# Kernel optimization log

Hardware: AMD Instinct MI355X
Metric: run time of the kernel (lower is better)

## Reference

```python
import jax, jax.numpy as jnp
import numpy as np

N_NODES = 100_000
N_EDGES = 1_600_000
N_GRAPHS = 256
IN_DIM, HID, HEADS, LAYERS = 480, 128, 4, 3
HEAD_DIM = HID // HEADS
NEG_SLOPE = 0.2
LN_EPS = 1e-5


def setup_inputs() -> dict:
    key = jax.random.key(0)
    ks = jax.random.split(key, 12)
    x = jax.random.normal(ks[0], (N_NODES, IN_DIM), dtype=jnp.float32)
    edge_index = jax.random.randint(ks[1], (2, N_EDGES), 0, N_NODES, dtype=jnp.int32)
    batch = jnp.sort(jax.random.randint(ks[2], (N_NODES,), 0, N_GRAPHS, dtype=jnp.int32))
    s_in = 1.0 / np.sqrt(IN_DIM)
    s_h = 1.0 / np.sqrt(HID)
    return {
        "x": x,
        "W_in": jax.random.uniform(ks[3], (IN_DIM, HID), jnp.float32, -s_in, s_in),
        "b_in": jax.random.uniform(ks[4], (HID,), jnp.float32, -s_in, s_in),
        "W_gat": jax.random.uniform(ks[5], (LAYERS, HID, HID), jnp.float32, -s_h, s_h),
        "att_src": jax.random.uniform(ks[6], (LAYERS, HEADS, HEAD_DIM), jnp.float32, -s_h, s_h),
        "att_dst": jax.random.uniform(ks[7], (LAYERS, HEADS, HEAD_DIM), jnp.float32, -s_h, s_h),
        "b_gat": jnp.zeros((LAYERS, HID), jnp.float32),
        "ln_g": jnp.ones((LAYERS, HID), jnp.float32),
        "ln_b": jnp.zeros((LAYERS, HID), jnp.float32),
        "edge_index": edge_index,
        "batch": batch,
    }


def _gat_conv(h_in, W, a_src, a_dst, bias, src, dst, n):
    # h: [N, H, D] per-head projected features
    h = (h_in @ W).reshape(n, HEADS, HEAD_DIM)
    asrc = jnp.sum(h * a_src, axis=-1)  # [N, H]
    adst = jnp.sum(h * a_dst, axis=-1)  # [N, H]
    e = jax.nn.leaky_relu(asrc[src] + adst[dst], NEG_SLOPE)  # [E, H]
    # scatter-softmax over incoming edges of each destination node
    emax = jax.ops.segment_max(e, dst, num_segments=n)  # [N, H]
    emax = jnp.where(jnp.isfinite(emax), emax, 0.0)
    ex = jnp.exp(e - emax[dst])
    denom = jax.ops.segment_sum(ex, dst, num_segments=n)
    alpha = ex / jnp.maximum(denom, 1e-16)[dst]  # [E, H]
    out = jax.ops.segment_sum(alpha[:, :, None] * h[src], dst, num_segments=n)
    return out.reshape(n, HID) + bias


def _layer_norm(x, g, b):
    mu = jnp.mean(x, axis=-1, keepdims=True)
    var = jnp.mean(jnp.square(x - mu), axis=-1, keepdims=True)
    return (x - mu) * jax.lax.rsqrt(var + LN_EPS) * g + b


def reference(x, W_in, b_in, W_gat, att_src, att_dst, b_gat, ln_g, ln_b, edge_index, batch):
    n = x.shape[0]
    # PyG GATConv default add_self_loops=True
    loop = jnp.arange(n, dtype=edge_index.dtype)
    src = jnp.concatenate([edge_index[0], loop])
    dst = jnp.concatenate([edge_index[1], loop])

    h = jax.nn.relu(x @ W_in + b_in)
    for l in range(LAYERS):
        residual = h
        h = _gat_conv(h, W_gat[l], att_src[l], att_dst[l], b_gat[l], src, dst, n)
        h = jax.nn.relu(_layer_norm(h, ln_g[l], ln_b[l]))
        # dropout omitted (eval mode)
        h = h + residual
    # global mean pool per graph
    sums = jax.ops.segment_sum(h, batch, num_segments=N_GRAPHS)
    cnt = jax.ops.segment_sum(jnp.ones((n,), h.dtype), batch, num_segments=N_GRAPHS)
    return sums / jnp.maximum(cnt, 1.0)[:, None]
```

## Files before the change

kernel.cpp:

```cpp
#include <hip/hip_runtime.h>
#include <hip/hip_bf16.h>

#define HID 128
#define NEG_SLOPE 0.2f
#define LN_EPS 1e-5f
#define SEG_CAP 8192

typedef __attribute__((ext_vector_type(8))) short short8;
typedef __attribute__((ext_vector_type(4))) float floatx4;

__device__ __forceinline__ float us2f(unsigned short u) {
    union { unsigned int i; float f; } c; c.i = ((unsigned int)u) << 16; return c.f;
}
__device__ __forceinline__ float lo2f(unsigned u) {
    union { unsigned int i; float f; } c; c.i = u << 16; return c.f;
}
__device__ __forceinline__ float hi2f(unsigned u) {
    union { unsigned int i; float f; } c; c.i = u & 0xffff0000u; return c.f;
}
__device__ __forceinline__ unsigned short f2us(float f) {
    union { float f; unsigned u; } c; c.f = f;
    unsigned r = c.u + 0x7FFF + ((c.u >> 16) & 1);
    return (unsigned short)(r >> 16);
}
__device__ __forceinline__ unsigned pack2(float a, float b) {
    return (unsigned)f2us(a) | ((unsigned)f2us(b) << 16);
}
__device__ __forceinline__ float ldw(const void* p, long i, int bf) {
    return bf ? us2f(((const unsigned short*)p)[i]) : ((const float*)p)[i];
}
__device__ __forceinline__ float lrelu(float x) { return x > 0.f ? x : NEG_SLOPE * x; }
__device__ __forceinline__ float wsum(float x) {
#pragma unroll
    for (int o = 32; o > 0; o >>= 1) x += __shfl_xor(x, o);
    return x;
}
__device__ __forceinline__ float pick4(float4 v, int h) {
    return h == 0 ? v.x : (h == 1 ? v.y : (h == 2 ? v.z : v.w));
}

__global__ void detect_kernel(const float* __restrict__ x, int* __restrict__ flag) {
    float v = x[threadIdx.x];
    int bad = (!(v == v)) || (fabsf(v) > 1e6f);
    unsigned long long m = __ballot(bad);
    if (threadIdx.x == 0) flag[0] = (m != 0ull) ? 1 : 0;
}

__global__ __launch_bounds__(256) void zero_int_kernel(int* p, int n) {
    int i = blockIdx.x * 256 + threadIdx.x;
    if (i < n) p[i] = 0;
}

__global__ __launch_bounds__(256) void bucket_hist_kernel(const int* __restrict__ dst, int E, int nb,
                                                          int* __restrict__ bucket_cnt) {
    __shared__ int hist[512];
    for (int i = threadIdx.x; i < nb; i += 256) hist[i] = 0;
    __syncthreads();
    const int base = blockIdx.x * 4096;
    const int end = min(base + 4096, E);
    for (int i = base + threadIdx.x; i < end; i += 256)
        atomicAdd(&hist[dst[i] >> 8], 1);
    __syncthreads();
    for (int i = threadIdx.x; i < nb; i += 256)
        if (hist[i]) atomicAdd(&bucket_cnt[i], hist[i]);
}

__global__ __launch_bounds__(512) void bucket_scan_kernel(const int* __restrict__ bucket_cnt,
                                                          int* __restrict__ bucket_base,
                                                          int* __restrict__ cursor,
                                                          int nb, int* __restrict__ row_ptr, int N) {
    __shared__ int sc[512];
    const int t = threadIdx.x;
    const int v = (t < nb) ? bucket_cnt[t] : 0;
    int x = v;
    sc[t] = x;
    __syncthreads();
    for (int o = 1; o < 512; o <<= 1) {
        const int y = (t >= o) ? sc[t - o] : 0;
        __syncthreads();
        x += y;
        sc[t] = x;
        __syncthreads();
    }
    if (t < nb) { bucket_base[t] = x - v; cursor[t] = x - v; }
    if (t == nb - 1) { bucket_base[nb] = x; row_ptr[N] = x; }
}

__global__ __launch_bounds__(256) void partition_kernel(const int* __restrict__ src, const int* __restrict__ dst,
                                                        int E, int nb, int* __restrict__ cursor,
                                                        unsigned long long* __restrict__ tmp) {
    __shared__ int hist[512];
    __shared__ int tbase[512];
    for (int i = threadIdx.x; i < nb; i += 256) hist[i] = 0;
    __syncthreads();
    const int base = blockIdx.x * 4096;
    const int end = min(base + 4096, E);
    int myd[16], mys[16], myr[16];
#pragma unroll
    for (int j = 0; j < 16; ++j) {
        const int i = base + threadIdx.x + j * 256;
        if (i < end) {
            const int d = dst[i];
            myd[j] = d;
            mys[j] = src[i];
            myr[j] = atomicAdd(&hist[d >> 8], 1);
        } else {
            myd[j] = -1;
        }
    }
    __syncthreads();
    for (int i = threadIdx.x; i < nb; i += 256) {
        const int hv = hist[i];
        tbase[i] = hv ? atomicAdd(&cursor[i], hv) : 0;
    }
    __syncthreads();
#pragma unroll
    for (int j = 0; j < 16; ++j) {
        if (myd[j] >= 0) {
            const int b = myd[j] >> 8;
            tmp[(size_t)tbase[b] + myr[j]] = ((unsigned long long)(unsigned)myd[j] << 32) | (unsigned)mys[j];
        }
    }
}

__global__ __launch_bounds__(256) void bucket_sort_kernel(const unsigned long long* __restrict__ tmp,
                                                          const int* __restrict__ bucket_base,
                                                          int* __restrict__ row_ptr, int* __restrict__ csr,
                                                          int N) {
    __shared__ int hist[256];
    __shared__ int sc[256];
    __shared__ int off[256];
    __shared__ int outb[SEG_CAP];
    const int b = blockIdx.x;
    const int node0 = b << 8;
    const int nn = min(256, N - node0);
    const int s0 = bucket_base[b], s1 = bucket_base[b + 1];
    const int cnt = s1 - s0;
    const int t = threadIdx.x;
    hist[t] = 0;
    __syncthreads();
    for (int i = s0 + t; i < s1; i += 256) {
        const int d = (int)(tmp[i] >> 32) - node0;
        atomicAdd(&hist[d], 1);
    }
    __syncthreads();
    const int v = hist[t];
    int x = v;
    sc[t] = x;
    __syncthreads();
    for (int o = 1; o < 256; o <<= 1) {
        const int y = (t >= o) ? sc[t - o] : 0;
        __syncthreads();
        x += y;
        sc[t] = x;
        __syncthreads();
    }
    off[t] = x - v;
    if (t < nn) row_ptr[node0 + t] = s0 + (x - v);
    hist[t] = 0;
    __syncthreads();
    if (cnt <= SEG_CAP) {
        for (int i = s0 + t; i < s1; i += 256) {
            const unsigned long long pr = tmp[i];
            const int d = (int)(pr >> 32) - node0;
            const int p = off[d] + atomicAdd(&hist[d], 1);
            outb[p] = (int)(unsigned)(pr & 0xffffffffu);
        }
        __syncthreads();
        for (int i = t; i < cnt; i += 256) csr[s0 + i] = outb[i];
    } else {
        for (int i = s0 + t; i < s1; i += 256) {
            const unsigned long long pr = tmp[i];
            const int d = (int)(pr >> 32) - node0;
            const int p = off[d] + atomicAdd(&hist[d], 1);
            csr[s0 + p] = (int)(unsigned)(pr & 0xffffffffu);
        }
    }
}

__global__ __launch_bounds__(256) void transpose_w_kernel(const void* __restrict__ W, long w_off, int K,
                                                          unsigned short* __restrict__ Wt,
                                                          const int* __restrict__ flagp) {
    const int bf = flagp[0];
    const int i = blockIdx.x * 256 + threadIdx.x;
    if (i >= 128 * K) return;
    const int n = i / K, k = i - n * K;
    const long s = w_off + (long)k * 128 + n;
    Wt[i] = bf ? ((const unsigned short*)W)[s] : f2us(((const float*)W)[s]);
}

template <int C_BF>
__global__ __launch_bounds__(256) void mfma_gemm_kernel(const void* __restrict__ Ap, int a_input,
                                                        const unsigned short* __restrict__ Bt,
                                                        const void* __restrict__ bias, long bias_off,
                                                        void* __restrict__ Cp,
                                                        int M, int K, int do_relu,
                                                        const int* __restrict__ flagp) {
    __shared__ unsigned short As[128 * 40];
    __shared__ unsigned short Bs[128 * 40];
    const int bf = flagp[0];
    const int a_bf = a_input ? bf : 2;
    const int t = threadIdx.x;
    const int bm = blockIdx.x * 128;
    const int lane = t & 63, wave = t >> 6;
    const int r = lane & 15, quad = lane >> 4;
    const int srow = t >> 1, skh = (t & 1) * 16;

    floatx4 acc[2][8];
#pragma unroll
    for (int mt = 0; mt < 2; ++mt)
#pragma unroll
        for (int nt = 0; nt < 8; ++nt)
#pragma unroll
            for (int q = 0; q < 4; ++q) acc[mt][nt][q] = 0.f;

    for (int k0 = 0; k0 < K; k0 += 32) {
        {
            const int grow = bm + srow;
            uint4 u0 = make_uint4(0, 0, 0, 0), u1 = u0;
            if (grow < M) {
                const long aidx = (long)grow * K + k0 + skh;
                if (a_bf == 1) {
                    const unsigned short* ap = (const unsigned short*)Ap + aidx;
                    u0 = ((const uint4*)ap)[0];
                    u1 = ((const uint4*)ap)[1];
                } else {
                    const float* ap = (const float*)Ap + aidx;
                    float4 f0 = ((const float4*)ap)[0];
                    float4 f1 = ((const float4*)ap)[1];
                    float4 f2 = ((const float4*)ap)[2];
                    float4 f3 = ((const float4*)ap)[3];
                    u0 = make_uint4(pack2(f0.x, f0.y), pack2(f0.z, f0.w), pack2(f1.x, f1.y), pack2(f1.z, f1.w));
                    u1 = make_uint4(pack2(f2.x, f2.y), pack2(f2.z, f2.w), pack2(f3.x, f3.y), pack2(f3.z, f3.w));
                }
            }
            *(uint4*)&As[srow * 40 + skh]     = u0;
            *(uint4*)&As[srow * 40 + skh + 8] = u1;
        }
        {
            const unsigned short* bp = Bt + (long)srow * K + k0 + skh;
            uint4 v0 = ((const uint4*)bp)[0];
            uint4 v1 = ((const uint4*)bp)[1];
            *(uint4*)&Bs[srow * 40 + skh]     = v0;
            *(uint4*)&Bs[srow * 40 + skh + 8] = v1;
        }
        __syncthreads();

        short8 afr[2];
        afr[0] = *(const short8*)&As[(wave * 32 + r) * 40 + quad * 8];
        afr[1] = *(const short8*)&As[(wave * 32 + 16 + r) * 40 + quad * 8];
#pragma unroll
        for (int nt = 0; nt < 8; ++nt) {
            short8 bfr = *(const short8*)&Bs[(nt * 16 + r) * 40 + quad * 8];
            acc[0][nt] = __builtin_amdgcn_mfma_f32_16x16x32_bf16(afr[0], bfr, acc[0][nt], 0, 0, 0);
            acc[1][nt] = __builtin_amdgcn_mfma_f32_16x16x32_bf16(afr[1], bfr, acc[1][nt], 0, 0, 0);
        }
        __syncthreads();
    }

    float bb[8];
#pragma unroll
    for (int nt = 0; nt < 8; ++nt) bb[nt] = bias ? ldw(bias, bias_off + nt * 16 + r, bf) : 0.f;

#pragma unroll
    for (int mt = 0; mt < 2; ++mt) {
        const int gr0 = bm + wave * 32 + mt * 16 + quad * 4;
#pragma unroll
        for (int reg = 0; reg < 4; ++reg) {
            const int grow = gr0 + reg;
            if (grow < M) {
#pragma unroll
                for (int nt = 0; nt < 8; ++nt) {
                    float v = acc[mt][nt][reg] + bb[nt];
                    if (do_relu) v = fmaxf(v, 0.f);
                    const long ci = (long)grow * HID + nt * 16 + r;
                    if (C_BF) ((unsigned short*)Cp)[ci] = f2us(v);
                    else      ((float*)Cp)[ci] = v;
                }
            }
        }
    }
}

__global__ __launch_bounds__(256) void attn_kernel(const unsigned short* __restrict__ hp,
                                                   const void* __restrict__ att_src,
                                                   const void* __restrict__ att_dst, long a_off,
                                                   float* __restrict__ asrc, float* __restrict__ adst,
                                                   int N, const int* __restrict__ flagp) {
    __shared__ float sA[128], sD[128];
    const int bf = flagp[0];
    const int t = threadIdx.x;
    if (t < 128) { sA[t] = ldw(att_src, a_off + t, bf); sD[t] = ldw(att_dst, a_off + t, bf); }
    __syncthreads();
    const int gid = blockIdx.x * 256 + t;
    if (gid >= N * 4) return;
    const int n = gid >> 2, hd = gid & 3;
    const unsigned short* p = hp + (size_t)n * HID + hd * 32;
    float s1 = 0.f, s2 = 0.f;
#pragma unroll
    for (int q = 0; q < 4; ++q) {
        uint4 v = ((const uint4*)p)[q];
        unsigned arr[4] = {v.x, v.y, v.z, v.w};
#pragma unroll
        for (int j = 0; j < 4; ++j) {
            const int k = q * 8 + j * 2;
            float lo = lo2f(arr[j]);
            float hi = hi2f(arr[j]);
            s1 += lo * sA[hd * 32 + k] + hi * sA[hd * 32 + k + 1];
            s2 += lo * sD[hd * 32 + k] + hi * sD[hd * 32 + k + 1];
        }
    }
    asrc[gid] = s1;
    adst[gid] = s2;
}

__global__ __launch_bounds__(256) void gat_kernel(float* __restrict__ h,
                                                  const unsigned short* __restrict__ hp,
                                                  const float* __restrict__ asrc,
                                                  const float* __restrict__ adst,
                                                  const int* __restrict__ row_ptr,
                                                  const int* __restrict__ csr,
                                                  const void* __restrict__ bgat,
                                                  const void* __restrict__ lng,
                                                  const void* __restrict__ lnb, long w_off,
                                                  int N, const int* __restrict__ flagp) {
    __shared__ uint2 ebuf[4][320];
    const int bf = flagp[0];
    const int lane = threadIdx.x & 63;
    const int wslot = threadIdx.x >> 6;
    const int half = lane >> 5;
    const int ll = lane & 31;
    const int head4 = ll >> 3;
    const int c0 = ll << 2;
    const int n = (blockIdx.x << 2) | wslot;
    if (n >= N) return;

    const int e0 = row_ptr[n], e1 = row_ptr[n + 1];
    const float4 ad4 = *(const float4*)(adst + (size_t)n * 4);
    const float4 as4 = *(const float4*)(asrc + (size_t)n * 4);
    float4 es;
    es.x = lrelu(as4.x + ad4.x); es.y = lrelu(as4.y + ad4.y);
    es.z = lrelu(as4.z + ad4.z); es.w = lrelu(as4.w + ad4.w);

    const uint2 us = *(const uint2*)(hp + (size_t)n * HID + c0);
    const float wself = half ? 0.f : 1.f;
    float4 acc;
    acc.x = wself * lo2f(us.x); acc.y = wself * hi2f(us.x);
    acc.z = wself * lo2f(us.y); acc.w = wself * hi2f(us.y);

    float4 dnp = make_float4(0.f, 0.f, 0.f, 0.f);
    uint2* eb = ebuf[wslot];

    for (int base = e0; base < e1; base += 64) {
        const int cnt = min(64, e1 - base);
        int s = 0;
        float4 ex4 = make_float4(0.f, 0.f, 0.f, 0.f);
        if (lane < cnt) {
            s = csr[base + lane];
            const float4 a = *(const float4*)(asrc + (size_t)s * 4);
            ex4.x = __expf(lrelu(a.x + ad4.x) - es.x);
            ex4.y = __expf(lrelu(a.y + ad4.y) - es.y);
            ex4.z = __expf(lrelu(a.z + ad4.z) - es.z);
            ex4.w = __expf(lrelu(a.w + ad4.w) - es.w);
            dnp.x += ex4.x; dnp.y += ex4.y; dnp.z += ex4.z; dnp.w += ex4.w;
        }
        const unsigned su = (unsigned)s;
        eb[lane * 5 + 0] = make_uint2(su, __float_as_uint(ex4.x));
        eb[lane * 5 + 1] = make_uint2(su, __float_as_uint(ex4.y));
        eb[lane * 5 + 2] = make_uint2(su, __float_as_uint(ex4.z));
        eb[lane * 5 + 3] = make_uint2(su, __float_as_uint(ex4.w));

        float4 aA = make_float4(0.f, 0.f, 0.f, 0.f);
        float4 aB = make_float4(0.f, 0.f, 0.f, 0.f);
        int i = half;
#define GAT_EDGE(idx, A)                                                      \
        {                                                                     \
            const uint2 q = eb[(idx) * 5 + head4];                            \
            const uint2 u = *(const uint2*)(hp + (size_t)q.x * HID + c0);     \
            const float wq = __uint_as_float(q.y);                            \
            A.x = fmaf(wq, lo2f(u.x), A.x);                                   \
            A.y = fmaf(wq, hi2f(u.x), A.y);                                   \
            A.z = fmaf(wq, lo2f(u.y), A.z);                                   \
            A.w = fmaf(wq, hi2f(u.y), A.w);                                   \
        }
        for (; i + 2 < cnt; i += 4) {
            GAT_EDGE(i, aA);
            GAT_EDGE(i + 2, aB);
        }
        for (; i < cnt; i += 2) GAT_EDGE(i, aA);
#undef GAT_EDGE
        acc.x += aA.x + aB.x; acc.y += aA.y + aB.y;
        acc.z += aA.z + aB.z; acc.w += aA.w + aB.w;
    }

    acc.x += __shfl_xor(acc.x, 32);
    acc.y += __shfl_xor(acc.y, 32);
    acc.z += __shfl_xor(acc.z, 32);
    acc.w += __shfl_xor(acc.w, 32);

    float4 dn;
    dn.x = wsum(dnp.x) + 1.f;
    dn.y = wsum(dnp.y) + 1.f;
    dn.z = wsum(dnp.z) + 1.f;
    dn.w = wsum(dnp.w) + 1.f;

    const float invd = 1.f / fmaxf(pick4(dn, head4), 1e-16f);
    acc.x *= invd; acc.y *= invd; acc.z *= invd; acc.w *= invd;
    acc.x += ldw(bgat, w_off + c0 + 0, bf);
    acc.y += ldw(bgat, w_off + c0 + 1, bf);
    acc.z += ldw(bgat, w_off + c0 + 2, bf);
    acc.w += ldw(bgat, w_off + c0 + 3, bf);

    const float mean = wsum(acc.x + acc.y + acc.z + acc.w) * (1.f / 256.f);
    const float d0 = acc.x - mean, d1 = acc.y - mean, d2 = acc.z - mean, d3 = acc.w - mean;
    const float var = wsum(d0 * d0 + d1 * d1 + d2 * d2 + d3 * d3) * (1.f / 256.f);
    const float rstd = rsqrtf(var + LN_EPS);
    float o0 = d0 * rstd * ldw(lng, w_off + c0 + 0, bf) + ldw(lnb, w_off + c0 + 0, bf);
    float o1 = d1 * rstd * ldw(lng, w_off + c0 + 1, bf) + ldw(lnb, w_off + c0 + 1, bf);
    float o2 = d2 * rstd * ldw(lng, w_off + c0 + 2, bf) + ldw(lnb, w_off + c0 + 2, bf);
    float o3 = d3 * rstd * ldw(lng, w_off + c0 + 3, bf) + ldw(lnb, w_off + c0 + 3, bf);
    o0 = fmaxf(o0, 0.f); o1 = fmaxf(o1, 0.f); o2 = fmaxf(o2, 0.f); o3 = fmaxf(o3, 0.f);

    if (half == 0) {
        const float4 r = *(const float4*)(h + (size_t)n * HID + c0);
        *(float4*)(h + (size_t)n * HID + c0) = make_float4(o0 + r.x, o1 + r.y, o2 + r.z, o3 + r.w);
    }
}

__global__ __launch_bounds__(256) void pool_kernel(const float* __restrict__ h, const int* __restrict__ batch,
                                                   void* __restrict__ out, int N,
                                                   const int* __restrict__ flagp) {
    const int g = blockIdx.x;
    int a = 0, b = N;
    while (a < b) { int mid = (a + b) >> 1; if (batch[mid] < g) a = mid + 1; else b = mid; }
    const int lo = a;
    b = N;
    while (a < b) { int mid = (a + b) >> 1; if (batch[mid] <= g) a = mid + 1; else b = mid; }
    const int hi = a;

    const int col = threadIdx.x & 127;
    const int half = threadIdx.x >> 7;
    float s = 0.f;
    for (int r = lo + half; r < hi; r += 2) s += h[(size_t)r * HID + col];
    __shared__ float part[128];
    if (half == 0) part[col] = s;
    __syncthreads();
    if (half == 1) {
        const float tot = part[col] + s;
        const float v = tot / fmaxf((float)(hi - lo), 1.f);
        if (flagp[0]) ((unsigned short*)out)[g * HID + col] = f2us(v);
        else          ((float*)out)[g * HID + col] = v;
    }
}

extern "C" void kernel_launch(void* const* d_in, const int* in_sizes, int n_in,
                              void* d_out, int out_size, void* d_ws, size_t ws_size,
                              hipStream_t stream) {
    const void* x     = d_in[0];
    const void* W_in  = d_in[1];
    const void* b_in  = d_in[2];
    const void* W_gat = d_in[3];
    const void* att_s = d_in[4];
    const void* att_d = d_in[5];
    const void* b_gat = d_in[6];
    const void* ln_g  = d_in[7];
    const void* ln_b  = d_in[8];
    const int* edge_index = (const int*)d_in[9];
    const int* batch      = (const int*)d_in[10];

    const int N = in_sizes[10];
    const int E = in_sizes[9] / 2;
    const int IN_DIM = in_sizes[0] / N;
    const int n_graphs = out_size / HID;

    const int* esrc = edge_index;
    const int* edst = edge_index + E;

    char* w = (char*)d_ws;
    auto carve = [&](size_t bytes) -> void* {
        void* p = (void*)w;
        w += (bytes + 255) & ~(size_t)255;
        return p;
    };
    int* flag             = (int*)carve(256);
    int* row_ptr          = (int*)carve((size_t)(N + 1) * 4);
    int* csr              = (int*)carve((size_t)E * 4);
    float* asrc           = (float*)carve((size_t)N * 4 * 4);
    float* adst           = (float*)carve((size_t)N * 4 * 4);
    int* bucket_cnt       = (int*)carve(512 * 4);
    int* bucket_base      = (int*)carve(513 * 4);
    int* cursor           = (int*)carve(512 * 4);
    unsigned short* Wt_in = (unsigned short*)carve((size_t)HID * IN_DIM * 2);
    unsigned short* Wt_g  = (unsigned short*)carve((size_t)HID * HID * 2);
    float* h              = (float*)carve((size_t)N * HID * 4);
    unsigned short* hp    = (unsigned short*)carve((size_t)N * HID * 2);
    unsigned long long* tmp = (unsigned long long*)h;
    (void)ws_size; (void)n_in;

    detect_kernel<<<1, 64, 0, stream>>>((const float*)x, flag);

    const int nb = (N + 255) >> 8;
    const int ntiles = (E + 4095) / 4096;
    zero_int_kernel<<<2, 256, 0, stream>>>(bucket_cnt, 512);
    bucket_hist_kernel<<<ntiles, 256, 0, stream>>>(edst, E, nb, bucket_cnt);
    bucket_scan_kernel<<<1, 512, 0, stream>>>(bucket_cnt, bucket_base, cursor, nb, row_ptr, N);
    partition_kernel<<<ntiles, 256, 0, stream>>>(esrc, edst, E, nb, cursor, tmp);
    bucket_sort_kernel<<<nb, 256, 0, stream>>>(tmp, bucket_base, row_ptr, csr, N);

    transpose_w_kernel<<<(HID * IN_DIM + 255) / 256, 256, 0, stream>>>(W_in, 0, IN_DIM, Wt_in, flag);
    mfma_gemm_kernel<0><<<(N + 127) / 128, 256, 0, stream>>>(x, 1, Wt_in, b_in, 0, h, N, IN_DIM, 1, flag);

    for (int l = 0; l < 3; ++l) {
        transpose_w_kernel<<<(HID * HID + 255) / 256, 256, 0, stream>>>(W_gat, (long)l * HID * HID, HID, Wt_g, flag);
        mfma_gemm_kernel<1><<<(N + 127) / 128, 256, 0, stream>>>(h, 0, Wt_g, nullptr, 0, hp, N, HID, 0, flag);
        attn_kernel<<<(N * 4 + 255) / 256, 256, 0, stream>>>(hp, att_s, att_d, (long)l * HID,
                                                             asrc, adst, N, flag);
        gat_kernel<<<(N + 3) / 4, 256, 0, stream>>>(h, hp, asrc, adst, row_ptr, csr,
                                                    b_gat, ln_g, ln_b, (long)l * HID, N, flag);
    }

    pool_kernel<<<n_graphs, 256, 0, stream>>>(h, batch, d_out, N, flag);
}
```

Measured before the change: 900.9 us.

## Map one node per half-wavefront in GAT aggregation kernel

The GAT aggregation kernel now assigns each destination node to a 32-lane half-wave instead of a full 64-lane wave, so each block processes eight nodes. Edge chunks shrink to 32, each half-wave processes every edge itself with a four-way unrolled accumulation, and the cross-half shuffle reduction plus the idle upper-half store are removed. The intent is to stop wasting half the lanes in the softmax and LayerNorm phases and to double the number of nodes in flight. The cost is longer per-node edge loops for high-degree nodes and divergence between the two nodes sharing a wave.

Result: faster. 809.8 us (-10.1%).

```diff
diff --git a/kernel.cpp b/kernel.cpp
--- a/kernel.cpp
+++ b/kernel.cpp
@@ -30,9 +30,9 @@
     return bf ? us2f(((const unsigned short*)p)[i]) : ((const float*)p)[i];
 }
 __device__ __forceinline__ float lrelu(float x) { return x > 0.f ? x : NEG_SLOPE * x; }
-__device__ __forceinline__ float wsum(float x) {
-#pragma unroll
-    for (int o = 32; o > 0; o >>= 1) x += __shfl_xor(x, o);
+__device__ __forceinline__ float wsum32(float x) {
+#pragma unroll
+    for (int o = 16; o > 0; o >>= 1) x += __shfl_xor(x, o);
     return x;
 }
 __device__ __forceinline__ float pick4(float4 v, int h) {
@@ -324,7 +324,7 @@
                                                   const void* __restrict__ lng,
                                                   const void* __restrict__ lnb, long w_off,
                                                   int N, const int* __restrict__ flagp) {
-    __shared__ uint2 ebuf[4][320];
+    __shared__ uint2 ebuf[8][160];
     const int bf = flagp[0];
     const int lane = threadIdx.x & 63;
     const int wslot = threadIdx.x >> 6;
@@ -332,7 +332,7 @@
     const int ll = lane & 31;
     const int head4 = ll >> 3;
     const int c0 = ll << 2;
-    const int n = (blockIdx.x << 2) | wslot;
+    const int n = (blockIdx.x << 3) | (wslot << 1) | half;
     if (n >= N) return;
 
     const int e0 = row_ptr[n], e1 = row_ptr[n + 1];
@@ -343,20 +343,19 @@
     es.z = lrelu(as4.z + ad4.z); es.w = lrelu(as4.w + ad4.w);
 
     const uint2 us = *(const uint2*)(hp + (size_t)n * HID + c0);
-    const float wself = half ? 0.f : 1.f;
     float4 acc;
-    acc.x = wself * lo2f(us.x); acc.y = wself * hi2f(us.x);
-    acc.z = wself * lo2f(us.y); acc.w = wself * hi2f(us.y);
+    acc.x = lo2f(us.x); acc.y = hi2f(us.x);
+    acc.z = lo2f(us.y); acc.w = hi2f(us.y);
 
     float4 dnp = make_float4(0.f, 0.f, 0.f, 0.f);
-    uint2* eb = ebuf[wslot];
-
-    for (int base = e0; base < e1; base += 64) {
-        const int cnt = min(64, e1 - base);
+    uint2* eb = ebuf[(wslot << 1) | half];
+
+    for (int base = e0; base < e1; base += 32) {
+        const int cnt = min(32, e1 - base);
         int s = 0;
         float4 ex4 = make_float4(0.f, 0.f, 0.f, 0.f);
-        if (lane < cnt) {
-            s = csr[base + lane];
+        if (ll < cnt) {
+            s = csr[base + ll];
             const float4 a = *(const float4*)(asrc + (size_t)s * 4);
             ex4.x = __expf(lrelu(a.x + ad4.x) - es.x);
             ex4.y = __expf(lrelu(a.y + ad4.y) - es.y);
@@ -365,14 +364,16 @@
             dnp.x += ex4.x; dnp.y += ex4.y; dnp.z += ex4.z; dnp.w += ex4.w;
         }
         const unsigned su = (unsigned)s;
-        eb[lane * 5 + 0] = make_uint2(su, __float_as_uint(ex4.x));
-        eb[lane * 5 + 1] = make_uint2(su, __float_as_uint(ex4.y));
-        eb[lane * 5 + 2] = make_uint2(su, __float_as_uint(ex4.z));
-        eb[lane * 5 + 3] = make_uint2(su, __float_as_uint(ex4.w));
+        eb[ll * 5 + 0] = make_uint2(su, __float_as_uint(ex4.x));
+        eb[ll * 5 + 1] = make_uint2(su, __float_as_uint(ex4.y));
+        eb[ll * 5 + 2] = make_uint2(su, __float_as_uint(ex4.z));
+        eb[ll * 5 + 3] = make_uint2(su, __float_as_uint(ex4.w));
 
         float4 aA = make_float4(0.f, 0.f, 0.f, 0.f);
         float4 aB = make_float4(0.f, 0.f, 0.f, 0.f);
-        int i = half;
+        float4 aC = make_float4(0.f, 0.f, 0.f, 0.f);
+        float4 aD = make_float4(0.f, 0.f, 0.f, 0.f);
+        int i = 0;
 #define GAT_EDGE(idx, A)                                                      \
         {                                                                     \
             const uint2 q = eb[(idx) * 5 + head4];                            \
@@ -383,26 +384,25 @@
             A.z = fmaf(wq, lo2f(u.y), A.z);                                   \
             A.w = fmaf(wq, hi2f(u.y), A.w);                                   \
         }
-        for (; i + 2 < cnt; i += 4) {
-            GAT_EDGE(i, aA);
-            GAT_EDGE(i + 2, aB);
-        }
-        for (; i < cnt; i += 2) GAT_EDGE(i, aA);
+        for (; i + 4 <= cnt; i += 4) {
+            GAT_EDGE(i + 0, aA);
+            GAT_EDGE(i + 1, aB);
+            GAT_EDGE(i + 2, aC);
+            GAT_EDGE(i + 3, aD);
+        }
+        for (; i < cnt; ++i) GAT_EDGE(i, aA);
 #undef GAT_EDGE
-        acc.x += aA.x + aB.x; acc.y += aA.y + aB.y;
-        acc.z += aA.z + aB.z; acc.w += aA.w + aB.w;
-    }
-
-    acc.x += __shfl_xor(acc.x, 32);
-    acc.y += __shfl_xor(acc.y, 32);
-    acc.z += __shfl_xor(acc.z, 32);
-    acc.w += __shfl_xor(acc.w, 32);
+        acc.x += (aA.x + aB.x) + (aC.x + aD.x);
+        acc.y += (aA.y + aB.y) + (aC.y + aD.y);
+        acc.z += (aA.z + aB.z) + (aC.z + aD.z);
+        acc.w += (aA.w + aB.w) + (aC.w + aD.w);
+    }
 
     float4 dn;
-    dn.x = wsum(dnp.x) + 1.f;
-    dn.y = wsum(dnp.y) + 1.f;
-    dn.z = wsum(dnp.z) + 1.f;
-    dn.w = wsum(dnp.w) + 1.f;
+    dn.x = wsum32(dnp.x) + 1.f;
+    dn.y = wsum32(dnp.y) + 1.f;
+    dn.z = wsum32(dnp.z) + 1.f;
+    dn.w = wsum32(dnp.w) + 1.f;
 
     const float invd = 1.f / fmaxf(pick4(dn, head4), 1e-16f);
     acc.x *= invd; acc.y *= invd; acc.z *= invd; acc.w *= invd;
@@ -411,9 +411,9 @@
     acc.z += ldw(bgat, w_off + c0 + 2, bf);
     acc.w += ldw(bgat, w_off + c0 + 3, bf);
 
-    const float mean = wsum(acc.x + acc.y + acc.z + acc.w) * (1.f / 256.f);
+    const float mean = wsum32(acc.x + acc.y + acc.z + acc.w) * (1.f / 128.f);
     const float d0 = acc.x - mean, d1 = acc.y - mean, d2 = acc.z - mean, d3 = acc.w - mean;
-    const float var = wsum(d0 * d0 + d1 * d1 + d2 * d2 + d3 * d3) * (1.f / 256.f);
+    const float var = wsum32(d0 * d0 + d1 * d1 + d2 * d2 + d3 * d3) * (1.f / 128.f);
     const float rstd = rsqrtf(var + LN_EPS);
     float o0 = d0 * rstd * ldw(lng, w_off + c0 + 0, bf) + ldw(lnb, w_off + c0 + 0, bf);
     float o1 = d1 * rstd * ldw(lng, w_off + c0 + 1, bf) + ldw(lnb, w_off + c0 + 1, bf);
@@ -421,10 +421,8 @@
     float o3 = d3 * rstd * ldw(lng, w_off + c0 + 3, bf) + ldw(lnb, w_off + c0 + 3, bf);
     o0 = fmaxf(o0, 0.f); o1 = fmaxf(o1, 0.f); o2 = fmaxf(o2, 0.f); o3 = fmaxf(o3, 0.f);
 
-    if (half == 0) {
-        const float4 r = *(const float4*)(h + (size_t)n * HID + c0);
-        *(float4*)(h + (size_t)n * HID + c0) = make_float4(o0 + r.x, o1 + r.y, o2 + r.z, o3 + r.w);
-    }
+    const float4 r = *(const float4*)(h + (size_t)n * HID + c0);
+    *(float4*)(h + (size_t)n * HID + c0) = make_float4(o0 + r.x, o1 + r.y, o2 + r.z, o3 + r.w);
 }
 
 __global__ __launch_bounds__(256) void pool_kernel(const float* __restrict__ h, const int* __restrict__ batch,
@@ -515,7 +513,7 @@
         mfma_gemm_kernel<1><<<(N + 127) / 128, 256, 0, stream>>>(h, 0, Wt_g, nullptr, 0, hp, N, HID, 0, flag);
         attn_kernel<<<(N * 4 + 255) / 256, 256, 0, stream>>>(hp, att_s, att_d, (long)l * HID,
                                                              asrc, adst, N, flag);
-        gat_kernel<<<(N + 3) / 4, 256, 0, stream>>>(h, hp, asrc, adst, row_ptr, csr,
+        gat_kernel<<<(N + 7) / 8, 256, 0, stream>>>(h, hp, asrc, adst, row_ptr, csr,
                                                     b_gat, ln_g, ln_b, (long)l * HID, N, flag);
     }
 
```
